# Optimization experiments

Hardware: AMD Instinct MI355X
Metric: run time of the kernel (lower is better)

Reference implementation:

```python
import jax, jax.numpy as jnp
import numpy as np

N = 4096
CIN = 128
COUT = 128
J = 2
DENSITY = 0.01  # ~40 nonzeros per Laplacian row


def _mask(k):
    m = (jax.random.uniform(k, (N, N)) < DENSITY).astype(jnp.float32)
    # Laplacians have nonzero diagonals; also guarantees no empty softmax rows
    return jnp.maximum(m, jnp.eye(N, dtype=jnp.float32))


def setup_inputs() -> dict:
    key = jax.random.key(0)
    ks = jax.random.split(key, 9)
    x = jax.random.normal(ks[0], (N, CIN), dtype=jnp.float32)
    Lup = _mask(ks[1])
    Ldown = _mask(ks[2])
    P = jax.random.normal(ks[3], (N, N), dtype=jnp.float32) / np.float32(np.sqrt(N))
    weight_irr = jax.random.normal(ks[4], (J, CIN, COUT), dtype=jnp.float32) * 0.05
    weight_sol = jax.random.normal(ks[5], (J, CIN, COUT), dtype=jnp.float32) * 0.05
    weight_har = jax.random.normal(ks[6], (CIN, COUT), dtype=jnp.float32) * 0.05
    att_irr = jax.random.normal(ks[7], (2 * J * COUT, 1), dtype=jnp.float32) * 0.05
    att_sol = jax.random.normal(ks[8], (2 * J * COUT, 1), dtype=jnp.float32) * 0.05
    return {"x": x, "Lup": Lup, "Ldown": Ldown, "P": P,
            "weight_irr": weight_irr, "weight_sol": weight_sol,
            "weight_har": weight_har, "att_irr": att_irr, "att_sol": att_sol}


def _masked_row_softmax(e, mask):
    # torch.sparse.softmax over the mask's nonzero pattern, dim=1, then to_dense
    on = mask > 0
    z = jnp.where(on, e, -jnp.inf)
    m = jnp.max(z, axis=1, keepdims=True)
    m = jnp.where(jnp.isfinite(m), m, 0.0)  # guard fully-masked rows
    p = jnp.exp(z - m)                      # exp(-inf)=0 off-pattern
    s = jnp.sum(p, axis=1, keepdims=True)
    s = jnp.where(s == 0, 1.0, s)
    return jnp.where(on, p / s, 0.0)


def _branch(x, weight, att, mask):
    j, cout = weight.shape[0], weight.shape[2]
    att_slice = j * cout
    h = jnp.einsum('ni,jio->jno', x, weight)         # [J, N, Cout]
    hf = h.reshape(-1, att_slice)                    # [N, J*Cout] (row-major, as torch)
    src = hf @ att[:att_slice]                       # [N, 1]
    dst = hf @ att[att_slice:]                       # [N, 1]
    e = jax.nn.leaky_relu(src + dst.T)               # [N, N], slope 0.01 (torch default)
    alpha = _masked_row_softmax(e, mask)             # [N, N]
    powers = [alpha]
    for _ in range(j - 1):
        powers.append(powers[-1] @ alpha)            # iterative matrix powers
    alpha_exp = jnp.stack(powers)                    # [J, N, N]
    # torch.sum with no dim: full reduction to a SCALAR (faithful to source)
    return jnp.sum(jnp.einsum('jnm,jmo->jno', alpha_exp, h))


def reference(x, Lup, Ldown, P, weight_irr, weight_sol, weight_har, att_irr, att_sol):
    z_irr = _branch(x, weight_irr, att_irr, Ldown)   # scalar
    z_sol = _branch(x, weight_sol, att_sol, Lup)     # scalar
    z_har = (P @ x) @ weight_har                     # [N, Cout]
    return z_irr + z_sol + z_har
```

## Files before the change

### kernel.cpp

```cpp
#include <hip/hip_runtime.h>

typedef __attribute__((ext_vector_type(8))) short short8b;
typedef __attribute__((ext_vector_type(4))) float f32x4;

#define NEG_SENTINEL (-1e30f)

constexpr int C_OFF    = 0;
constexpr int C2_OFF   = 8192;
constexpr int SC_OFF   = 16384;
constexpr int FLAG_I   = 16390;
constexpr int ZERO_N   = 16448;
constexpr int V_OFF    = 16448;
constexpr int NP_OFF   = 19008;
constexpr int SRC_OFF  = 100928;
constexpr int RM_OFF   = 117312;
constexpr int RS_OFF   = 125504;
constexpr int XBT_OFF  = 666176;
constexpr int TP_OFF   = 928320;
constexpr int BM_OFF   = 5122624;

__device__ __forceinline__ unsigned short f2bf(float f) {
  unsigned int u = __float_as_uint(f);
  u += 0x7FFFu + ((u >> 16) & 1u);
  return (unsigned short)(u >> 16);
}
__device__ __forceinline__ float bf2f(unsigned short b) {
  return __uint_as_float(((unsigned int)b) << 16);
}
__device__ __forceinline__ float scrub(float v) {
  unsigned int u = __float_as_uint(v);
  return ((u & 0x7F800000u) == 0x7F800000u) ? 0.f : v;
}

__global__ __launch_bounds__(128) void k_vvec(const void* __restrict__ xin,
                                              const void* __restrict__ w_irr,
                                              const void* __restrict__ w_sol,
                                              const void* __restrict__ att_irr,
                                              const void* __restrict__ att_sol,
                                              int* __restrict__ flagp,
                                              float* __restrict__ vvec) {
  __shared__ int sdet[128];
  int t = threadIdx.x;
  unsigned int ef = (((const unsigned int*)xin)[t] >> 7) & 0xFFu;
  sdet[t] = (ef >= 100u && ef <= 150u) ? 1 : 0;
  __syncthreads();
  for (int d = 64; d > 0; d >>= 1) { if (t < d) sdet[t] += sdet[t + d]; __syncthreads(); }
  int f = (sdet[0] >= 96) ? 1 : 0;
  if (blockIdx.x == 0 && t == 0) *flagp = f;
  int bx = blockIdx.x;
  int b = bx / 10, rem = bx % 10, j = rem / 5, tt = rem % 5;
  const void* Wv = (b == 0 ? w_irr : w_sol);
  const void* Av = (b == 0 ? att_irr : att_sol);
  int i = t;
  float s = 0.f;
  if (f) {
    const unsigned short* Wr = (const unsigned short*)Wv + (size_t)j * 16384 + (size_t)i * 128;
    const unsigned short* Ar = (const unsigned short*)Av + tt * 128;
    for (int o = 0; o < 128; o += 8) {
      uint4 wq = *(const uint4*)(Wr + o);
      unsigned int ww[4] = {wq.x, wq.y, wq.z, wq.w};
      float cf[8];
      if (tt < 4) {
        uint4 aq = *(const uint4*)(Ar + o);
        unsigned int aa[4] = {aq.x, aq.y, aq.z, aq.w};
#pragma unroll
        for (int u = 0; u < 4; ++u) {
          cf[2 * u] = bf2f((unsigned short)(aa[u] & 0xFFFFu));
          cf[2 * u + 1] = bf2f((unsigned short)(aa[u] >> 16));
        }
      } else {
#pragma unroll
        for (int e = 0; e < 8; ++e) cf[e] = 1.0f;
      }
#pragma unroll
      for (int u = 0; u < 4; ++u) {
        s += bf2f((unsigned short)(ww[u] & 0xFFFFu)) * cf[2 * u];
        s += bf2f((unsigned short)(ww[u] >> 16)) * cf[2 * u + 1];
      }
    }
  } else {
    const float* Wr = (const float*)Wv + (size_t)j * 16384 + (size_t)i * 128;
    const float* Ar = (const float*)Av + tt * 128;
    for (int o = 0; o < 128; o += 4) {
      float4 wq = *(const float4*)(Wr + o);
      float4 aq = {1.f, 1.f, 1.f, 1.f};
      if (tt < 4) aq = *(const float4*)(Ar + o);
      s += wq.x * aq.x + wq.y * aq.y + wq.z * aq.z + wq.w * aq.w;
    }
  }
  vvec[bx * 128 + i] = s;
}

__global__ __launch_bounds__(256) void k_prep(const void* __restrict__ xin,
                                              const int* __restrict__ flag,
                                              const float* __restrict__ vvec,
                                              unsigned short* __restrict__ xbT,
                                              float* __restrict__ np,
                                              float* __restrict__ srcdst) {
  __shared__ __align__(16) float ldsx[64 * 130];
  __shared__ __align__(16) float ldsv[2560];
  __shared__ float ldsp[4 * 1280];
  __shared__ float npl[1280];
  int f = *flag;
  int t = threadIdx.x, nb = blockIdx.x * 64;
  for (int q = 0; q < 16; ++q) {
    int idx = q * 256 + t;
    int row = idx >> 6, cp = idx & 63;
    float vx, vy;
    if (f) {
      unsigned int u = ((const unsigned int*)xin)[(size_t)(nb + row) * 64 + cp];
      vx = bf2f((unsigned short)(u & 0xFFFFu));
      vy = bf2f((unsigned short)(u >> 16));
    } else {
      float2 v = ((const float2*)xin)[(size_t)(nb + row) * 64 + cp];
      vx = v.x; vy = v.y;
    }
    ldsx[row * 130 + cp * 2] = vx;
    ldsx[row * 130 + cp * 2 + 1] = vy;
  }
  for (int q = 0; q < 10; ++q) { int idx = q * 256 + t; ldsv[idx] = vvec[idx]; }
  __syncthreads();
  for (int q = 0; q < 32; ++q) {
    int idx = q * 256 + t;
    int c = idx >> 6, n = idx & 63;
    xbT[(size_t)c * 4096 + nb + n] = f2bf(ldsx[n * 130 + c]);
  }
  int row = t & 63, qq = t >> 6, i0 = qq * 32;
  float acc[20];
#pragma unroll
  for (int k = 0; k < 20; ++k) acc[k] = 0.f;
  for (int i = i0; i < i0 + 32; i += 2) {
    float2 xv = *(const float2*)&ldsx[row * 130 + i];
#pragma unroll
    for (int k = 0; k < 20; ++k) {
      float2 vk = *(const float2*)&ldsv[k * 128 + i];
      acc[k] += xv.x * vk.x + xv.y * vk.y;
    }
  }
#pragma unroll
  for (int k = 0; k < 20; ++k) ldsp[qq * 1280 + row * 20 + k] = acc[k];
  __syncthreads();
  for (int rep = 0; rep < 5; ++rep) {
    int idx = rep * 256 + t;
    int k = idx >> 6, rr = idx & 63;
    float s = ldsp[rr * 20 + k] + ldsp[1280 + rr * 20 + k] +
              ldsp[2560 + rr * 20 + k] + ldsp[3840 + rr * 20 + k];
    npl[k * 64 + rr] = s;
    np[(size_t)k * 4096 + nb + rr] = s;
  }
  __syncthreads();
  {
    int b = t >> 7, j = (t >> 6) & 1, kind = (t >> 5) & 1, q = t & 31;
    int bl = q * 2;
    int r = j * 2048 + (nb >> 1) + q;
    int kidx = b * 10 + j * 5 + kind * 2;
    float val = npl[kidx * 64 + bl] + npl[(kidx + 1) * 64 + bl + 1];
    srcdst[b * 8192 + kind * 4096 + r] = val;
  }
}

__global__ __launch_bounds__(256) void k_mask(const void* __restrict__ Ldown,
                                              const void* __restrict__ Lup,
                                              const int* __restrict__ flag,
                                              unsigned char* __restrict__ bm) {
  __shared__ __align__(16) unsigned char lb[4096];
  int f = *flag;
  int b = blockIdx.y;
  const void* mask = b ? Lup : Ldown;
  int t = threadIdx.x;
  size_t wg = (size_t)blockIdx.x * 4096;
  if (f) {
    const uint4* in4 = (const uint4*)mask;
#pragma unroll
    for (int k = 0; k < 16; ++k) {
      size_t bi = wg + k * 256 + t;
      uint4 v = in4[bi];
      unsigned int by = 0;
      by |= ((v.x & 0xFFFFu) != 0u ? 1u : 0u) << 0;
      by |= ((v.x >> 16) != 0u ? 1u : 0u) << 1;
      by |= ((v.y & 0xFFFFu) != 0u ? 1u : 0u) << 2;
      by |= ((v.y >> 16) != 0u ? 1u : 0u) << 3;
      by |= ((v.z & 0xFFFFu) != 0u ? 1u : 0u) << 4;
      by |= ((v.z >> 16) != 0u ? 1u : 0u) << 5;
      by |= ((v.w & 0xFFFFu) != 0u ? 1u : 0u) << 6;
      by |= ((v.w >> 16) != 0u ? 1u : 0u) << 7;
      lb[k * 256 + t] = (unsigned char)by;
    }
  } else {
    const uint4* in4 = (const uint4*)mask;
#pragma unroll
    for (int k = 0; k < 16; ++k) {
      size_t bi = wg + k * 256 + t;
      uint4 v0 = in4[2 * bi], v1 = in4[2 * bi + 1];
      unsigned int by = 0;
      by |= (v0.x != 0u ? 1u : 0u) << 0;
      by |= (v0.y != 0u ? 1u : 0u) << 1;
      by |= (v0.z != 0u ? 1u : 0u) << 2;
      by |= (v0.w != 0u ? 1u : 0u) << 3;
      by |= (v1.x != 0u ? 1u : 0u) << 4;
      by |= (v1.y != 0u ? 1u : 0u) << 5;
      by |= (v1.z != 0u ? 1u : 0u) << 6;
      by |= (v1.w != 0u ? 1u : 0u) << 7;
      lb[k * 256 + t] = (unsigned char)by;
    }
  }
  __syncthreads();
  ((uint4*)(bm + (size_t)b * 2097152 + wg))[t] = ((const uint4*)lb)[t];
}

__global__ __launch_bounds__(256) void k_soft(float* __restrict__ ws) {
  const unsigned char* bm = (const unsigned char*)(ws + BM_OFF);
  int b = blockIdx.y, t = threadIdx.x;
  int wid = t >> 6, l = t & 63;
  const float* srcp = ws + SRC_OFF + b * 8192;
  const float* dstp = srcp + 4096;
#pragma unroll
  for (int rr = 0; rr < 2; ++rr) {
    int r = blockIdx.x * 8 + wid * 2 + rr;
    unsigned long long hm =
        ((const unsigned long long*)(bm + ((size_t)b * 4096 + r) * 512))[l];
    float srcr = srcp[r];
    float ev[8];
    int mv[8];
    int nh = 0;
    float mx = NEG_SENTINEL, sm = 0.f;
    unsigned long long mm = hm;
    while (mm) {
      int bit = __builtin_ctzll(mm); mm &= mm - 1;
      int m = l * 64 + bit;
      float e = srcr + dstp[m];
      e = (e >= 0.f) ? e : 0.01f * e;
      if (nh < 8) { ev[nh] = e; mv[nh] = m; }
      ++nh;
      if (e > mx) { sm = sm * __expf(mx - e) + 1.f; mx = e; }
      else        { sm += __expf(e - mx); }
    }
    for (int d = 1; d < 64; d <<= 1) {
      float om = __shfl_xor(mx, d);
      float os = __shfl_xor(sm, d);
      float M = fmaxf(mx, om);
      sm = sm * __expf(mx - M) + os * __expf(om - M);
      mx = M;
    }
    if (l == 0) {
      ws[RM_OFF + b * 4096 + r] = mx;
      ws[RS_OFF + b * 4096 + r] = sm;
    }
    float inv = 1.0f / sm;
    int cap = (nh < 8) ? nh : 8;
    for (int i = 0; i < cap; ++i)
      atomicAdd(&ws[C_OFF + b * 4096 + mv[i]], __expf(ev[i] - mx) * inv);
    if (nh > 8) {
      int skip = 8;
      mm = hm;
      while (mm) {
        int bit = __builtin_ctzll(mm); mm &= mm - 1;
        if (skip > 0) { --skip; continue; }
        int m = l * 64 + bit;
        float e = srcr + dstp[m];
        e = (e >= 0.f) ? e : 0.01f * e;
        atomicAdd(&ws[C_OFF + b * 4096 + m], __expf(e - mx) * inv);
      }
    }
  }
}

__global__ __launch_bounds__(256) void k_c2(float* __restrict__ ws) {
  const unsigned char* bm = (const unsigned char*)(ws + BM_OFF);
  int b = blockIdx.y, t = threadIdx.x;
  int wid = t >> 6, l = t & 63;
  const float* srcp = ws + SRC_OFF + b * 8192;
  const float* dstp = srcp + 4096;
#pragma unroll
  for (int rr = 0; rr < 2; ++rr) {
    int r = blockIdx.x * 8 + wid * 2 + rr;
    unsigned long long hm =
        ((const unsigned long long*)(bm + ((size_t)b * 4096 + r) * 512))[l];
    float srcr = srcp[r];
    float rm = ws[RM_OFF + b * 4096 + r];
    float w = ws[C_OFF + b * 4096 + r] / ws[RS_OFF + b * 4096 + r];
    while (hm) {
      int bit = __builtin_ctzll(hm); hm &= hm - 1;
      int m = l * 64 + bit;
      float e = srcr + dstp[m];
      e = (e >= 0.f) ? e : 0.01f * e;
      atomicAdd(&ws[C2_OFF + b * 4096 + m], __expf(e - rm) * w);
    }
  }
}

__global__ __launch_bounds__(256) void k_scalar(float* __restrict__ ws) {
  int b = blockIdx.x, t = threadIdx.x;
  const float* cb  = ws + C_OFF  + b * 4096;
  const float* c2b = ws + C2_OFF + b * 4096;
  const float* hr0 = ws + NP_OFF + (b * 10 + 4) * 4096;
  const float* hr1 = ws + NP_OFF + (b * 10 + 9) * 4096;
  double acc = 0.0;
  for (int m = t; m < 4096; m += 256)
    acc += (double)scrub(cb[m]) * (double)scrub(hr0[m]) +
           (double)scrub(c2b[m]) * (double)scrub(hr1[m]);
  __shared__ double sd[256];
  sd[t] = acc;
  __syncthreads();
  for (int s = 128; s > 0; s >>= 1) { if (t < s) sd[t] += sd[t + s]; __syncthreads(); }
  if (t == 0) atomicAdd(&ws[SC_OFF], (float)sd[0]);
}

__global__ __launch_bounds__(256) void k_gemm1(const void* __restrict__ P,
                                               const unsigned short* __restrict__ xbT,
                                               const int* __restrict__ flag,
                                               float* __restrict__ TP) {
  __shared__ __align__(16) unsigned short a_lds[64 * 40];
  __shared__ __align__(16) unsigned short b_lds[128 * 40];
  int f = *flag;
  const int mt = blockIdx.x & 63, ks = blockIdx.x >> 6;
  const int mb = mt * 64;
  const int t = threadIdx.x;
  const int w = t >> 6, l = t & 63, quad = l >> 4, lr = l & 15;
  f32x4 acc[8] = {};
  const int arow = t >> 2, akq = (t & 3) << 3;
  const int bn = t >> 1, bh = (t & 1) << 4;
  const int k0 = ks * 512;
  uint4 aU, bU0, bU1;
#define LOADT(IT)                                                              \
  {                                                                            \
    const int kb = k0 + (IT) * 32;                                             \
    if (f) {                                                                   \
      aU = *(const uint4*)((const unsigned short*)P +                          \
                           (size_t)(mb + arow) * 4096 + kb + akq);             \
    } else {                                                                   \
      const float* pa = (const float*)P + (size_t)(mb + arow) * 4096 + kb + akq; \
      float4 f0 = *(const float4*)pa;                                          \
      float4 f1 = *(const float4*)(pa + 4);                                    \
      unsigned short u[8] = {f2bf(f0.x), f2bf(f0.y), f2bf(f0.z), f2bf(f0.w),   \
                             f2bf(f1.x), f2bf(f1.y), f2bf(f1.z), f2bf(f1.w)};  \
      aU = *(const uint4*)u;                                                   \
    }                                                                          \
    const unsigned short* src = xbT + (size_t)bn * 4096 + kb + bh;             \
    bU0 = *(const uint4*)src;                                                  \
    bU1 = *(const uint4*)(src + 8);                                            \
  }
  LOADT(0);
  for (int it = 0; it < 16; ++it) {
    *(uint4*)&a_lds[arow * 40 + akq] = aU;
    *(uint4*)&b_lds[bn * 40 + bh] = bU0;
    *(uint4*)&b_lds[bn * 40 + bh + 8] = bU1;
    __syncthreads();
    if (it < 15) LOADT(it + 1);
    short8b af = *(short8b*)&a_lds[(w * 16 + lr) * 40 + quad * 8];
#pragma unroll
    for (int nt = 0; nt < 8; ++nt) {
      short8b bf = *(short8b*)&b_lds[(nt * 16 + lr) * 40 + quad * 8];
      acc[nt] = __builtin_amdgcn_mfma_f32_16x16x32_bf16(af, bf, acc[nt], 0, 0, 0);
    }
    if (it < 15) __syncthreads();
  }
#undef LOADT
  float* Tp = TP + (size_t)ks * 524288;
#pragma unroll
  for (int nt = 0; nt < 8; ++nt)
#pragma unroll
    for (int rr = 0; rr < 4; ++rr) {
      int row = mb + w * 16 + quad * 4 + rr;
      int col = nt * 16 + lr;
      Tp[(size_t)row * 128 + col] = acc[nt][rr];
    }
}

__global__ __launch_bounds__(256) void k_gemm2(const float* __restrict__ TP,
                                               const void* __restrict__ W,
                                               const float* __restrict__ ws,
                                               void* __restrict__ outv) {
  __shared__ float tl[16 * 128];
  int f = ((const int*)ws)[FLAG_I];
  int t = threadIdx.x;
  int rb = blockIdx.x * 16;
  for (int q = 0; q < 2; ++q) {
    int vi = q * 256 + t;
    size_t base = (size_t)rb * 128 + (size_t)vi * 4;
    float4 s = {0.f, 0.f, 0.f, 0.f};
#pragma unroll
    for (int p = 0; p < 8; ++p) {
      float4 v = *(const float4*)&TP[(size_t)p * 524288 + base];
      s.x += v.x; s.y += v.y; s.z += v.z; s.w += v.w;
    }
    *(float4*)&tl[vi * 4] = s;
  }
  __syncthreads();
  int col = t & 127, rg = t >> 7;
  int r0 = rg * 8;
  float acc[8] = {};
  for (int k = 0; k < 128; k += 4) {
    float w0, w1, w2, w3;
    if (f) {
      const unsigned short* W16 = (const unsigned short*)W;
      w0 = bf2f(W16[(k + 0) * 128 + col]); w1 = bf2f(W16[(k + 1) * 128 + col]);
      w2 = bf2f(W16[(k + 2) * 128 + col]); w3 = bf2f(W16[(k + 3) * 128 + col]);
    } else {
      const float* W32 = (const float*)W;
      w0 = W32[(k + 0) * 128 + col]; w1 = W32[(k + 1) * 128 + col];
      w2 = W32[(k + 2) * 128 + col]; w3 = W32[(k + 3) * 128 + col];
    }
#pragma unroll
    for (int rr = 0; rr < 8; ++rr) {
      float4 tv = *(const float4*)&tl[(r0 + rr) * 128 + k];
      acc[rr] += tv.x * w0 + tv.y * w1 + tv.z * w2 + tv.w * w3;
    }
  }
  float s = scrub(ws[SC_OFF]);
#pragma unroll
  for (int rr = 0; rr < 8; ++rr) {
    size_t oi = (size_t)(rb + r0 + rr) * 128 + col;
    float v = s + acc[rr];
    if (f) ((unsigned short*)outv)[oi] = f2bf(v);
    else   ((float*)outv)[oi] = v;
  }
}

extern "C" void kernel_launch(void* const* d_in, const int* in_sizes, int n_in,
                              void* d_out, int out_size, void* d_ws, size_t ws_size,
                              hipStream_t stream) {
  const void* x       = d_in[0];
  const void* Lup     = d_in[1];
  const void* Ldown   = d_in[2];
  const void* P       = d_in[3];
  const void* w_irr   = d_in[4];
  const void* w_sol   = d_in[5];
  const void* w_har   = d_in[6];
  const void* att_irr = d_in[7];
  const void* att_sol = d_in[8];
  float* ws = (float*)d_ws;

  hipMemsetAsync(d_ws, 0, (size_t)ZERO_N * sizeof(float), stream);
  k_vvec  <<<20, 128, 0, stream>>>(x, w_irr, w_sol, att_irr, att_sol,
                                   (int*)ws + FLAG_I, ws + V_OFF);
  k_prep  <<<64, 256, 0, stream>>>(x, (int*)ws + FLAG_I, ws + V_OFF,
                                   (unsigned short*)(ws + XBT_OFF), ws + NP_OFF,
                                   ws + SRC_OFF);
  k_gemm1 <<<512, 256, 0, stream>>>(P, (const unsigned short*)(ws + XBT_OFF),
                                    (int*)ws + FLAG_I, ws + TP_OFF);
  k_mask  <<<dim3(512, 2), 256, 0, stream>>>(Ldown, Lup, (int*)ws + FLAG_I,
                                             (unsigned char*)(ws + BM_OFF));
  k_soft  <<<dim3(512, 2), 256, 0, stream>>>(ws);
  k_c2    <<<dim3(512, 2), 256, 0, stream>>>(ws);
  k_scalar<<<2, 256, 0, stream>>>(ws);
  k_gemm2 <<<256, 256, 0, stream>>>(ws + TP_OFF, w_har, ws, d_out);
}
```

Baseline: 320.8 us.

## Fuse all stages into one persistent kernel with software grid barriers

```diff
diff --git a/kernel.cpp b/kernel.cpp
--- a/kernel.cpp
+++ b/kernel.cpp
@@ -4,20 +4,23 @@
 typedef __attribute__((ext_vector_type(4))) float f32x4;
 
 #define NEG_SENTINEL (-1e30f)
+#define MAGIC 0x5A17C0DE
+constexpr int NB = 256;
 
 constexpr int C_OFF    = 0;
 constexpr int C2_OFF   = 8192;
-constexpr int SC_OFF   = 16384;
-constexpr int FLAG_I   = 16390;
-constexpr int ZERO_N   = 16448;
+constexpr int BAR_CNT  = 16388;
+constexpr int BAR_GEN  = 16389;
+constexpr int BAR_MAG  = 16390;
 constexpr int V_OFF    = 16448;
 constexpr int NP_OFF   = 19008;
 constexpr int SRC_OFF  = 100928;
 constexpr int RM_OFF   = 117312;
 constexpr int RS_OFF   = 125504;
-constexpr int XBT_OFF  = 666176;
-constexpr int TP_OFF   = 928320;
-constexpr int BM_OFF   = 5122624;
+constexpr int XBT_OFF  = 133696;
+constexpr int T_OFF    = 395840;
+constexpr int TP_OFF   = 920128;
+constexpr int BM_OFF   = 3017280;
 
 __device__ __forceinline__ unsigned short f2bf(float f) {
   unsigned int u = __float_as_uint(f);
@@ -32,417 +35,425 @@
   return ((u & 0x7F800000u) == 0x7F800000u) ? 0.f : v;
 }
 
-__global__ __launch_bounds__(128) void k_vvec(const void* __restrict__ xin,
-                                              const void* __restrict__ w_irr,
-                                              const void* __restrict__ w_sol,
-                                              const void* __restrict__ att_irr,
-                                              const void* __restrict__ att_sol,
-                                              int* __restrict__ flagp,
-                                              float* __restrict__ vvec) {
-  __shared__ int sdet[128];
-  int t = threadIdx.x;
-  unsigned int ef = (((const unsigned int*)xin)[t] >> 7) & 0xFFu;
-  sdet[t] = (ef >= 100u && ef <= 150u) ? 1 : 0;
+__device__ __forceinline__ void gbar(int* ib) {
   __syncthreads();
-  for (int d = 64; d > 0; d >>= 1) { if (t < d) sdet[t] += sdet[t + d]; __syncthreads(); }
-  int f = (sdet[0] >= 96) ? 1 : 0;
-  if (blockIdx.x == 0 && t == 0) *flagp = f;
-  int bx = blockIdx.x;
-  int b = bx / 10, rem = bx % 10, j = rem / 5, tt = rem % 5;
-  const void* Wv = (b == 0 ? w_irr : w_sol);
-  const void* Av = (b == 0 ? att_irr : att_sol);
-  int i = t;
-  float s = 0.f;
-  if (f) {
-    const unsigned short* Wr = (const unsigned short*)Wv + (size_t)j * 16384 + (size_t)i * 128;
-    const unsigned short* Ar = (const unsigned short*)Av + tt * 128;
-    for (int o = 0; o < 128; o += 8) {
-      uint4 wq = *(const uint4*)(Wr + o);
-      unsigned int ww[4] = {wq.x, wq.y, wq.z, wq.w};
-      float cf[8];
-      if (tt < 4) {
-        uint4 aq = *(const uint4*)(Ar + o);
-        unsigned int aa[4] = {aq.x, aq.y, aq.z, aq.w};
+  if (threadIdx.x == 0) {
+    __threadfence();
+    int g = __hip_atomic_load(&ib[BAR_GEN], __ATOMIC_RELAXED, __HIP_MEMORY_SCOPE_AGENT);
+    int a = __hip_atomic_fetch_add(&ib[BAR_CNT], 1, __ATOMIC_ACQ_REL, __HIP_MEMORY_SCOPE_AGENT);
+    if (a == NB - 1) {
+      __hip_atomic_store(&ib[BAR_CNT], 0, __ATOMIC_RELAXED, __HIP_MEMORY_SCOPE_AGENT);
+      __hip_atomic_store(&ib[BAR_GEN], g + 1, __ATOMIC_RELEASE, __HIP_MEMORY_SCOPE_AGENT);
+    } else {
+      while (__hip_atomic_load(&ib[BAR_GEN], __ATOMIC_ACQUIRE, __HIP_MEMORY_SCOPE_AGENT) == g)
+        __builtin_amdgcn_s_sleep(2);
+    }
+  }
+  __syncthreads();
+}
+
+__global__ __launch_bounds__(256, 1) void k_all(
+    const void* __restrict__ x, const void* __restrict__ Lup,
+    const void* __restrict__ Ldown, const void* __restrict__ P,
+    const void* __restrict__ w_irr, const void* __restrict__ w_sol,
+    const void* __restrict__ w_har, const void* __restrict__ att_irr,
+    const void* __restrict__ att_sol, float* __restrict__ ws,
+    void* __restrict__ outv) {
+  __shared__ __align__(16) unsigned char smem[69632];
+  int* ib = (int*)ws;
+  const int bid = blockIdx.x, t = threadIdx.x;
+
+  if (bid == 0 && t == 0) {
+    __hip_atomic_store(&ib[BAR_CNT], 0, __ATOMIC_RELAXED, __HIP_MEMORY_SCOPE_AGENT);
+    __hip_atomic_store(&ib[BAR_GEN], 0, __ATOMIC_RELAXED, __HIP_MEMORY_SCOPE_AGENT);
+    __threadfence();
+    __hip_atomic_store(&ib[BAR_MAG], MAGIC, __ATOMIC_RELEASE, __HIP_MEMORY_SCOPE_AGENT);
+  }
+
+  int flag;
+  {
+    int* sd = (int*)smem;
+    unsigned int ef = (((const unsigned int*)x)[t & 127] >> 7) & 0xFFu;
+    sd[t] = (ef >= 100u && ef <= 150u) ? 1 : 0;
+    __syncthreads();
+    for (int d = 128; d > 0; d >>= 1) { if (t < d) sd[t] += sd[t + d]; __syncthreads(); }
+    flag = (sd[0] >= 192) ? 1 : 0;
+    __syncthreads();
+  }
+
+  if (bid < 20 && t < 128) {
+    int b = bid / 10, rem = bid % 10, j = rem / 5, tt = rem % 5;
+    const void* Wv = (b == 0 ? w_irr : w_sol);
+    const void* Av = (b == 0 ? att_irr : att_sol);
+    float s = 0.f;
+    if (flag) {
+      const unsigned short* Wr = (const unsigned short*)Wv + (size_t)j * 16384 + (size_t)t * 128;
+      const unsigned short* Ar = (const unsigned short*)Av + tt * 128;
+      for (int o = 0; o < 128; o += 8) {
+        uint4 wq = *(const uint4*)(Wr + o);
+        unsigned int ww[4] = {wq.x, wq.y, wq.z, wq.w};
+        float cf[8];
+        if (tt < 4) {
+          uint4 aq = *(const uint4*)(Ar + o);
+          unsigned int aa[4] = {aq.x, aq.y, aq.z, aq.w};
+#pragma unroll
+          for (int u = 0; u < 4; ++u) {
+            cf[2 * u] = bf2f((unsigned short)(aa[u] & 0xFFFFu));
+            cf[2 * u + 1] = bf2f((unsigned short)(aa[u] >> 16));
+          }
+        } else {
+#pragma unroll
+          for (int e = 0; e < 8; ++e) cf[e] = 1.0f;
+        }
 #pragma unroll
         for (int u = 0; u < 4; ++u) {
-          cf[2 * u] = bf2f((unsigned short)(aa[u] & 0xFFFFu));
-          cf[2 * u + 1] = bf2f((unsigned short)(aa[u] >> 16));
+          s += bf2f((unsigned short)(ww[u] & 0xFFFFu)) * cf[2 * u];
+          s += bf2f((unsigned short)(ww[u] >> 16)) * cf[2 * u + 1];
+        }
+      }
+    } else {
+      const float* Wr = (const float*)Wv + (size_t)j * 16384 + (size_t)t * 128;
+      const float* Ar = (const float*)Av + tt * 128;
+      for (int o = 0; o < 128; o += 4) {
+        float4 wq = *(const float4*)(Wr + o);
+        float4 aq = {1.f, 1.f, 1.f, 1.f};
+        if (tt < 4) aq = *(const float4*)(Ar + o);
+        s += wq.x * aq.x + wq.y * aq.y + wq.z * aq.z + wq.w * aq.w;
+      }
+    }
+    ws[V_OFF + bid * 128 + t] = s;
+  }
+  if (bid >= 64 && bid < 128) ws[(bid - 64) * 256 + t] = 0.f;
+
+  if (t == 0) {
+    while (__hip_atomic_load(&ib[BAR_MAG], __ATOMIC_ACQUIRE, __HIP_MEMORY_SCOPE_AGENT) != MAGIC)
+      __builtin_amdgcn_s_sleep(2);
+  }
+  __syncthreads();
+  gbar(ib);
+
+  if (bid < 64) {
+    float* ldsx = (float*)smem;
+    float* ldsv = (float*)(smem + 33280);
+    float* ldsp = (float*)(smem + 43520);
+    float* npl  = (float*)(smem + 64000);
+    int nb = bid * 64;
+    for (int q = 0; q < 16; ++q) {
+      int idx = q * 256 + t;
+      int row = idx >> 6, cp = idx & 63;
+      float vx, vy;
+      if (flag) {
+        unsigned int u = ((const unsigned int*)x)[(size_t)(nb + row) * 64 + cp];
+        vx = bf2f((unsigned short)(u & 0xFFFFu));
+        vy = bf2f((unsigned short)(u >> 16));
+      } else {
+        float2 v = ((const float2*)x)[(size_t)(nb + row) * 64 + cp];
+        vx = v.x; vy = v.y;
+      }
+      ldsx[row * 130 + cp * 2] = vx;
+      ldsx[row * 130 + cp * 2 + 1] = vy;
+    }
+    for (int q = 0; q < 10; ++q) { int idx = q * 256 + t; ldsv[idx] = ws[V_OFF + idx]; }
+    __syncthreads();
+    unsigned short* xbT = (unsigned short*)(ws + XBT_OFF);
+    for (int q = 0; q < 32; ++q) {
+      int idx = q * 256 + t;
+      int c = idx >> 6, n = idx & 63;
+      xbT[(size_t)c * 4096 + nb + n] = f2bf(ldsx[n * 130 + c]);
+    }
+    int row = t & 63, qq = t >> 6, i0 = qq * 32;
+    float acc[20];
+#pragma unroll
+    for (int k = 0; k < 20; ++k) acc[k] = 0.f;
+    for (int i = i0; i < i0 + 32; i += 2) {
+      float2 xv = *(const float2*)&ldsx[row * 130 + i];
+#pragma unroll
+      for (int k = 0; k < 20; ++k) {
+        float2 vk = *(const float2*)&ldsv[k * 128 + i];
+        acc[k] += xv.x * vk.x + xv.y * vk.y;
+      }
+    }
+#pragma unroll
+    for (int k = 0; k < 20; ++k) ldsp[qq * 1280 + row * 20 + k] = acc[k];
+    __syncthreads();
+    for (int rep = 0; rep < 5; ++rep) {
+      int idx = rep * 256 + t;
+      int k = idx >> 6, rr = idx & 63;
+      float s = ldsp[rr * 20 + k] + ldsp[1280 + rr * 20 + k] +
+                ldsp[2560 + rr * 20 + k] + ldsp[3840 + rr * 20 + k];
+      npl[k * 64 + rr] = s;
+      ws[NP_OFF + (size_t)k * 4096 + nb + rr] = s;
+    }
+    __syncthreads();
+    {
+      int b = t >> 7, j = (t >> 6) & 1, kind = (t >> 5) & 1, q = t & 31;
+      int bl = q * 2;
+      int r = j * 2048 + (nb >> 1) + q;
+      int kidx = b * 10 + j * 5 + kind * 2;
+      float val = npl[kidx * 64 + bl] + npl[(kidx + 1) * 64 + bl + 1];
+      ws[SRC_OFF + b * 8192 + kind * 4096 + r] = val;
+    }
+  } else {
+    unsigned char* bm = (unsigned char*)(ws + BM_OFF);
+    for (int u = (bid - 64) * 256 + t; u < 262144; u += 192 * 256) {
+      int mb = u >> 17;
+      int rem = u & 131071;
+      const void* mask = mb ? Lup : Ldown;
+      unsigned int ob[4];
+      if (flag) {
+        const uint4* in4 = (const uint4*)mask + (size_t)rem * 16;
+#pragma unroll
+        for (int w4 = 0; w4 < 4; ++w4) {
+          unsigned int byts = 0;
+#pragma unroll
+          for (int bb = 0; bb < 4; ++bb) {
+            uint4 v = in4[w4 * 4 + bb];
+            unsigned int by = 0;
+            by |= ((v.x & 0xFFFFu) != 0u ? 1u : 0u) << 0;
+            by |= ((v.x >> 16) != 0u ? 1u : 0u) << 1;
+            by |= ((v.y & 0xFFFFu) != 0u ? 1u : 0u) << 2;
+            by |= ((v.y >> 16) != 0u ? 1u : 0u) << 3;
+            by |= ((v.z & 0xFFFFu) != 0u ? 1u : 0u) << 4;
+            by |= ((v.z >> 16) != 0u ? 1u : 0u) << 5;
+            by |= ((v.w & 0xFFFFu) != 0u ? 1u : 0u) << 6;
+            by |= ((v.w >> 16) != 0u ? 1u : 0u) << 7;
+            byts |= by << (8 * bb);
+          }
+          ob[w4] = byts;
         }
       } else {
-#pragma unroll
-        for (int e = 0; e < 8; ++e) cf[e] = 1.0f;
-      }
-#pragma unroll
-      for (int u = 0; u < 4; ++u) {
-        s += bf2f((unsigned short)(ww[u] & 0xFFFFu)) * cf[2 * u];
-        s += bf2f((unsigned short)(ww[u] >> 16)) * cf[2 * u + 1];
-      }
-    }
-  } else {
-    const float* Wr = (const float*)Wv + (size_t)j * 16384 + (size_t)i * 128;
-    const float* Ar = (const float*)Av + tt * 128;
-    for (int o = 0; o < 128; o += 4) {
-      float4 wq = *(const float4*)(Wr + o);
-      float4 aq = {1.f, 1.f, 1.f, 1.f};
-      if (tt < 4) aq = *(const float4*)(Ar + o);
-      s += wq.x * aq.x + wq.y * aq.y + wq.z * aq.z + wq.w * aq.w;
-    }
-  }
-  vvec[bx * 128 + i] = s;
-}
-
-__global__ __launch_bounds__(256) void k_prep(const void* __restrict__ xin,
-                                              const int* __restrict__ flag,
-                                              const float* __restrict__ vvec,
-                                              unsigned short* __restrict__ xbT,
-                                              float* __restrict__ np,
-                                              float* __restrict__ srcdst) {
-  __shared__ __align__(16) float ldsx[64 * 130];
-  __shared__ __align__(16) float ldsv[2560];
-  __shared__ float ldsp[4 * 1280];
-  __shared__ float npl[1280];
-  int f = *flag;
-  int t = threadIdx.x, nb = blockIdx.x * 64;
-  for (int q = 0; q < 16; ++q) {
-    int idx = q * 256 + t;
-    int row = idx >> 6, cp = idx & 63;
-    float vx, vy;
-    if (f) {
-      unsigned int u = ((const unsigned int*)xin)[(size_t)(nb + row) * 64 + cp];
-      vx = bf2f((unsigned short)(u & 0xFFFFu));
-      vy = bf2f((unsigned short)(u >> 16));
-    } else {
-      float2 v = ((const float2*)xin)[(size_t)(nb + row) * 64 + cp];
-      vx = v.x; vy = v.y;
-    }
-    ldsx[row * 130 + cp * 2] = vx;
-    ldsx[row * 130 + cp * 2 + 1] = vy;
-  }
-  for (int q = 0; q < 10; ++q) { int idx = q * 256 + t; ldsv[idx] = vvec[idx]; }
-  __syncthreads();
-  for (int q = 0; q < 32; ++q) {
-    int idx = q * 256 + t;
-    int c = idx >> 6, n = idx & 63;
-    xbT[(size_t)c * 4096 + nb + n] = f2bf(ldsx[n * 130 + c]);
-  }
-  int row = t & 63, qq = t >> 6, i0 = qq * 32;
-  float acc[20];
-#pragma unroll
-  for (int k = 0; k < 20; ++k) acc[k] = 0.f;
-  for (int i = i0; i < i0 + 32; i += 2) {
-    float2 xv = *(const float2*)&ldsx[row * 130 + i];
-#pragma unroll
-    for (int k = 0; k < 20; ++k) {
-      float2 vk = *(const float2*)&ldsv[k * 128 + i];
-      acc[k] += xv.x * vk.x + xv.y * vk.y;
-    }
-  }
-#pragma unroll
-  for (int k = 0; k < 20; ++k) ldsp[qq * 1280 + row * 20 + k] = acc[k];
-  __syncthreads();
-  for (int rep = 0; rep < 5; ++rep) {
-    int idx = rep * 256 + t;
-    int k = idx >> 6, rr = idx & 63;
-    float s = ldsp[rr * 20 + k] + ldsp[1280 + rr * 20 + k] +
-              ldsp[2560 + rr * 20 + k] + ldsp[3840 + rr * 20 + k];
-    npl[k * 64 + rr] = s;
-    np[(size_t)k * 4096 + nb + rr] = s;
-  }
-  __syncthreads();
-  {
-    int b = t >> 7, j = (t >> 6) & 1, kind = (t >> 5) & 1, q = t & 31;
-    int bl = q * 2;
-    int r = j * 2048 + (nb >> 1) + q;
-    int kidx = b * 10 + j * 5 + kind * 2;
-    float val = npl[kidx * 64 + bl] + npl[(kidx + 1) * 64 + bl + 1];
-    srcdst[b * 8192 + kind * 4096 + r] = val;
-  }
-}
-
-__global__ __launch_bounds__(256) void k_mask(const void* __restrict__ Ldown,
-                                              const void* __restrict__ Lup,
-                                              const int* __restrict__ flag,
-                                              unsigned char* __restrict__ bm) {
-  __shared__ __align__(16) unsigned char lb[4096];
-  int f = *flag;
-  int b = blockIdx.y;
-  const void* mask = b ? Lup : Ldown;
-  int t = threadIdx.x;
-  size_t wg = (size_t)blockIdx.x * 4096;
-  if (f) {
-    const uint4* in4 = (const uint4*)mask;
-#pragma unroll
-    for (int k = 0; k < 16; ++k) {
-      size_t bi = wg + k * 256 + t;
-      uint4 v = in4[bi];
-      unsigned int by = 0;
-      by |= ((v.x & 0xFFFFu) != 0u ? 1u : 0u) << 0;
-      by |= ((v.x >> 16) != 0u ? 1u : 0u) << 1;
-      by |= ((v.y & 0xFFFFu) != 0u ? 1u : 0u) << 2;
-      by |= ((v.y >> 16) != 0u ? 1u : 0u) << 3;
-      by |= ((v.z & 0xFFFFu) != 0u ? 1u : 0u) << 4;
-      by |= ((v.z >> 16) != 0u ? 1u : 0u) << 5;
-      by |= ((v.w & 0xFFFFu) != 0u ? 1u : 0u) << 6;
-      by |= ((v.w >> 16) != 0u ? 1u : 0u) << 7;
-      lb[k * 256 + t] = (unsigned char)by;
-    }
-  } else {
-    const uint4* in4 = (const uint4*)mask;
-#pragma unroll
-    for (int k = 0; k < 16; ++k) {
-      size_t bi = wg + k * 256 + t;
-      uint4 v0 = in4[2 * bi], v1 = in4[2 * bi + 1];
-      unsigned int by = 0;
-      by |= (v0.x != 0u ? 1u : 0u) << 0;
-      by |= (v0.y != 0u ? 1u : 0u) << 1;
-      by |= (v0.z != 0u ? 1u : 0u) << 2;
-      by |= (v0.w != 0u ? 1u : 0u) << 3;
-      by |= (v1.x != 0u ? 1u : 0u) << 4;
-      by |= (v1.y != 0u ? 1u : 0u) << 5;
-      by |= (v1.z != 0u ? 1u : 0u) << 6;
-      by |= (v1.w != 0u ? 1u : 0u) << 7;
-      lb[k * 256 + t] = (unsigned char)by;
-    }
-  }
-  __syncthreads();
-  ((uint4*)(bm + (size_t)b * 2097152 + wg))[t] = ((const uint4*)lb)[t];
-}
-
-__global__ __launch_bounds__(256) void k_soft(float* __restrict__ ws) {
-  const unsigned char* bm = (const unsigned char*)(ws + BM_OFF);
-  int b = blockIdx.y, t = threadIdx.x;
-  int wid = t >> 6, l = t & 63;
-  const float* srcp = ws + SRC_OFF + b * 8192;
-  const float* dstp = srcp + 4096;
-#pragma unroll
-  for (int rr = 0; rr < 2; ++rr) {
-    int r = blockIdx.x * 8 + wid * 2 + rr;
-    unsigned long long hm =
-        ((const unsigned long long*)(bm + ((size_t)b * 4096 + r) * 512))[l];
-    float srcr = srcp[r];
-    float ev[8];
-    int mv[8];
-    int nh = 0;
-    float mx = NEG_SENTINEL, sm = 0.f;
-    unsigned long long mm = hm;
-    while (mm) {
-      int bit = __builtin_ctzll(mm); mm &= mm - 1;
-      int m = l * 64 + bit;
-      float e = srcr + dstp[m];
-      e = (e >= 0.f) ? e : 0.01f * e;
-      if (nh < 8) { ev[nh] = e; mv[nh] = m; }
-      ++nh;
-      if (e > mx) { sm = sm * __expf(mx - e) + 1.f; mx = e; }
-      else        { sm += __expf(e - mx); }
-    }
-    for (int d = 1; d < 64; d <<= 1) {
-      float om = __shfl_xor(mx, d);
-      float os = __shfl_xor(sm, d);
-      float M = fmaxf(mx, om);
-      sm = sm * __expf(mx - M) + os * __expf(om - M);
-      mx = M;
-    }
-    if (l == 0) {
-      ws[RM_OFF + b * 4096 + r] = mx;
-      ws[RS_OFF + b * 4096 + r] = sm;
-    }
-    float inv = 1.0f / sm;
-    int cap = (nh < 8) ? nh : 8;
-    for (int i = 0; i < cap; ++i)
-      atomicAdd(&ws[C_OFF + b * 4096 + mv[i]], __expf(ev[i] - mx) * inv);
-    if (nh > 8) {
-      int skip = 8;
-      mm = hm;
+        const uint4* in4 = (const uint4*)mask + (size_t)rem * 32;
+#pragma unroll
+        for (int w4 = 0; w4 < 4; ++w4) {
+          unsigned int byts = 0;
+#pragma unroll
+          for (int bb = 0; bb < 4; ++bb) {
+            uint4 v0 = in4[w4 * 8 + bb * 2], v1 = in4[w4 * 8 + bb * 2 + 1];
+            unsigned int by = (v0.x != 0u ? 1u : 0u) | ((v0.y != 0u ? 1u : 0u) << 1) |
+                              ((v0.z != 0u ? 1u : 0u) << 2) | ((v0.w != 0u ? 1u : 0u) << 3) |
+                              ((v1.x != 0u ? 1u : 0u) << 4) | ((v1.y != 0u ? 1u : 0u) << 5) |
+                              ((v1.z != 0u ? 1u : 0u) << 6) | ((v1.w != 0u ? 1u : 0u) << 7);
+            byts |= by << (8 * bb);
+          }
+          ob[w4] = byts;
+        }
+      }
+      uint4 o; o.x = ob[0]; o.y = ob[1]; o.z = ob[2]; o.w = ob[3];
+      ((uint4*)bm)[u] = o;
+    }
+  }
+  gbar(ib);
+
+  {
+    const unsigned char* bm = (const unsigned char*)(ws + BM_OFF);
+    int wid = t >> 6, l = t & 63;
+    for (int rr = 0; rr < 8; ++rr) {
+      int GR = bid * 32 + wid * 8 + rr;
+      int b = GR >> 12, r = GR & 4095;
+      unsigned long long hm =
+          ((const unsigned long long*)(bm + ((size_t)b * 4096 + r) * 512))[l];
+      const float* srcp = ws + SRC_OFF + b * 8192;
+      const float* dstp = srcp + 4096;
+      float srcr = srcp[r];
+      float ev[8]; int mv[8]; int nh = 0;
+      float mx = NEG_SENTINEL, sm = 0.f;
+      unsigned long long mm = hm;
       while (mm) {
         int bit = __builtin_ctzll(mm); mm &= mm - 1;
-        if (skip > 0) { --skip; continue; }
         int m = l * 64 + bit;
         float e = srcr + dstp[m];
         e = (e >= 0.f) ? e : 0.01f * e;
-        atomicAdd(&ws[C_OFF + b * 4096 + m], __expf(e - mx) * inv);
-      }
-    }
-  }
-}
-
-__global__ __launch_bounds__(256) void k_c2(float* __restrict__ ws) {
-  const unsigned char* bm = (const unsigned char*)(ws + BM_OFF);
-  int b = blockIdx.y, t = threadIdx.x;
-  int wid = t >> 6, l = t & 63;
-  const float* srcp = ws + SRC_OFF + b * 8192;
-  const float* dstp = srcp + 4096;
-#pragma unroll
-  for (int rr = 0; rr < 2; ++rr) {
-    int r = blockIdx.x * 8 + wid * 2 + rr;
-    unsigned long long hm =
-        ((const unsigned long long*)(bm + ((size_t)b * 4096 + r) * 512))[l];
-    float srcr = srcp[r];
-    float rm = ws[RM_OFF + b * 4096 + r];
-    float w = ws[C_OFF + b * 4096 + r] / ws[RS_OFF + b * 4096 + r];
-    while (hm) {
-      int bit = __builtin_ctzll(hm); hm &= hm - 1;
-      int m = l * 64 + bit;
-      float e = srcr + dstp[m];
-      e = (e >= 0.f) ? e : 0.01f * e;
-      atomicAdd(&ws[C2_OFF + b * 4096 + m], __expf(e - rm) * w);
-    }
-  }
-}
-
-__global__ __launch_bounds__(256) void k_scalar(float* __restrict__ ws) {
-  int b = blockIdx.x, t = threadIdx.x;
-  const float* cb  = ws + C_OFF  + b * 4096;
-  const float* c2b = ws + C2_OFF + b * 4096;
-  const float* hr0 = ws + NP_OFF + (b * 10 + 4) * 4096;
-  const float* hr1 = ws + NP_OFF + (b * 10 + 9) * 4096;
-  double acc = 0.0;
-  for (int m = t; m < 4096; m += 256)
-    acc += (double)scrub(cb[m]) * (double)scrub(hr0[m]) +
-           (double)scrub(c2b[m]) * (double)scrub(hr1[m]);
-  __shared__ double sd[256];
-  sd[t] = acc;
+        if (nh < 8) { ev[nh] = e; mv[nh] = m; }
+        ++nh;
+        if (e > mx) { sm = sm * __expf(mx - e) + 1.f; mx = e; }
+        else        { sm += __expf(e - mx); }
+      }
+      for (int d = 1; d < 64; d <<= 1) {
+        float om = __shfl_xor(mx, d);
+        float os = __shfl_xor(sm, d);
+        float M = fmaxf(mx, om);
+        sm = sm * __expf(mx - M) + os * __expf(om - M);
+        mx = M;
+      }
+      if (l == 0) {
+        ws[RM_OFF + b * 4096 + r] = mx;
+        ws[RS_OFF + b * 4096 + r] = sm;
+      }
+      float inv = 1.0f / sm;
+      int cap = (nh < 8) ? nh : 8;
+      for (int i = 0; i < cap; ++i)
+        atomicAdd(&ws[C_OFF + b * 4096 + mv[i]], __expf(ev[i] - mx) * inv);
+      if (nh > 8) {
+        int skip = 8;
+        mm = hm;
+        while (mm) {
+          int bit = __builtin_ctzll(mm); mm &= mm - 1;
+          if (skip > 0) { --skip; continue; }
+          int m = l * 64 + bit;
+          float e = srcr + dstp[m];
+          e = (e >= 0.f) ? e : 0.01f * e;
+          atomicAdd(&ws[C_OFF + b * 4096 + m], __expf(e - mx) * inv);
+        }
+      }
+    }
+  }
   __syncthreads();
-  for (int s = 128; s > 0; s >>= 1) { if (t < s) sd[t] += sd[t + s]; __syncthreads(); }
-  if (t == 0) atomicAdd(&ws[SC_OFF], (float)sd[0]);
-}
-
-__global__ __launch_bounds__(256) void k_gemm1(const void* __restrict__ P,
-                                               const unsigned short* __restrict__ xbT,
-                                               const int* __restrict__ flag,
-                                               float* __restrict__ TP) {
-  __shared__ __align__(16) unsigned short a_lds[64 * 40];
-  __shared__ __align__(16) unsigned short b_lds[128 * 40];
-  int f = *flag;
-  const int mt = blockIdx.x & 63, ks = blockIdx.x >> 6;
-  const int mb = mt * 64;
-  const int t = threadIdx.x;
-  const int w = t >> 6, l = t & 63, quad = l >> 4, lr = l & 15;
-  f32x4 acc[8] = {};
-  const int arow = t >> 2, akq = (t & 3) << 3;
-  const int bn = t >> 1, bh = (t & 1) << 4;
-  const int k0 = ks * 512;
-  uint4 aU, bU0, bU1;
+  {
+    unsigned short* a_lds = (unsigned short*)smem;
+    unsigned short* b_lds = (unsigned short*)(smem + 5120);
+    const unsigned short* xbT = (const unsigned short*)(ws + XBT_OFF);
+    const int mt = bid & 63, ks = bid >> 6;
+    const int mb = mt * 64;
+    const int w = t >> 6, l = t & 63, quad = l >> 4, lr = l & 15;
+    f32x4 acc[8] = {};
+    const int arow = t >> 2, akq = (t & 3) << 3;
+    const int bn = t >> 1, bh = (t & 1) << 4;
+    const int k0 = ks * 1024;
+    uint4 aU, bU0, bU1;
 #define LOADT(IT)                                                              \
   {                                                                            \
     const int kb = k0 + (IT) * 32;                                             \
-    if (f) {                                                                   \
+    if (flag) {                                                                \
       aU = *(const uint4*)((const unsigned short*)P +                          \
                            (size_t)(mb + arow) * 4096 + kb + akq);             \
     } else {                                                                   \
       const float* pa = (const float*)P + (size_t)(mb + arow) * 4096 + kb + akq; \
       float4 f0 = *(const float4*)pa;                                          \
       float4 f1 = *(const float4*)(pa + 4);                                    \
-      unsigned short u[8] = {f2bf(f0.x), f2bf(f0.y), f2bf(f0.z), f2bf(f0.w),   \
-                             f2bf(f1.x), f2bf(f1.y), f2bf(f1.z), f2bf(f1.w)};  \
-      aU = *(const uint4*)u;                                                   \
+      unsigned short uu[8] = {f2bf(f0.x), f2bf(f0.y), f2bf(f0.z), f2bf(f0.w),  \
+                              f2bf(f1.x), f2bf(f1.y), f2bf(f1.z), f2bf(f1.w)}; \
+      aU = *(const uint4*)uu;                                                  \
     }                                                                          \
     const unsigned short* src = xbT + (size_t)bn * 4096 + kb + bh;             \
     bU0 = *(const uint4*)src;                                                  \
     bU1 = *(const uint4*)(src + 8);                                            \
   }
-  LOADT(0);
-  for (int it = 0; it < 16; ++it) {
-    *(uint4*)&a_lds[arow * 40 + akq] = aU;
-    *(uint4*)&b_lds[bn * 40 + bh] = bU0;
-    *(uint4*)&b_lds[bn * 40 + bh + 8] = bU1;
-    __syncthreads();
-    if (it < 15) LOADT(it + 1);
-    short8b af = *(short8b*)&a_lds[(w * 16 + lr) * 40 + quad * 8];
-#pragma unroll
-    for (int nt = 0; nt < 8; ++nt) {
-      short8b bf = *(short8b*)&b_lds[(nt * 16 + lr) * 40 + quad * 8];
-      acc[nt] = __builtin_amdgcn_mfma_f32_16x16x32_bf16(af, bf, acc[nt], 0, 0, 0);
-    }
-    if (it < 15) __syncthreads();
-  }
+    LOADT(0);
+    for (int it = 0; it < 32; ++it) {
+      *(uint4*)&a_lds[arow * 40 + akq] = aU;
+      *(uint4*)&b_lds[bn * 40 + bh] = bU0;
+      *(uint4*)&b_lds[bn * 40 + bh + 8] = bU1;
+      __syncthreads();
+      if (it < 31) LOADT(it + 1);
+      short8b af = *(short8b*)&a_lds[(w * 16 + lr) * 40 + quad * 8];
+#pragma unroll
+      for (int nt = 0; nt < 8; ++nt) {
+        short8b bf = *(short8b*)&b_lds[(nt * 16 + lr) * 40 + quad * 8];
+        acc[nt] = __builtin_amdgcn_mfma_f32_16x16x32_bf16(af, bf, acc[nt], 0, 0, 0);
+      }
+      if (it < 31) __syncthreads();
+    }
 #undef LOADT
-  float* Tp = TP + (size_t)ks * 524288;
-#pragma unroll
-  for (int nt = 0; nt < 8; ++nt)
-#pragma unroll
-    for (int rr = 0; rr < 4; ++rr) {
-      int row = mb + w * 16 + quad * 4 + rr;
-      int col = nt * 16 + lr;
-      Tp[(size_t)row * 128 + col] = acc[nt][rr];
-    }
-}
-
-__global__ __launch_bounds__(256) void k_gemm2(const float* __restrict__ TP,
-                                               const void* __restrict__ W,
-                                               const float* __restrict__ ws,
-                                               void* __restrict__ outv) {
-  __shared__ float tl[16 * 128];
-  int f = ((const int*)ws)[FLAG_I];
-  int t = threadIdx.x;
-  int rb = blockIdx.x * 16;
-  for (int q = 0; q < 2; ++q) {
-    int vi = q * 256 + t;
-    size_t base = (size_t)rb * 128 + (size_t)vi * 4;
-    float4 s = {0.f, 0.f, 0.f, 0.f};
-#pragma unroll
-    for (int p = 0; p < 8; ++p) {
-      float4 v = *(const float4*)&TP[(size_t)p * 524288 + base];
-      s.x += v.x; s.y += v.y; s.z += v.z; s.w += v.w;
-    }
-    *(float4*)&tl[vi * 4] = s;
-  }
-  __syncthreads();
-  int col = t & 127, rg = t >> 7;
-  int r0 = rg * 8;
-  float acc[8] = {};
-  for (int k = 0; k < 128; k += 4) {
-    float w0, w1, w2, w3;
-    if (f) {
-      const unsigned short* W16 = (const unsigned short*)W;
-      w0 = bf2f(W16[(k + 0) * 128 + col]); w1 = bf2f(W16[(k + 1) * 128 + col]);
-      w2 = bf2f(W16[(k + 2) * 128 + col]); w3 = bf2f(W16[(k + 3) * 128 + col]);
-    } else {
-      const float* W32 = (const float*)W;
-      w0 = W32[(k + 0) * 128 + col]; w1 = W32[(k + 1) * 128 + col];
-      w2 = W32[(k + 2) * 128 + col]; w3 = W32[(k + 3) * 128 + col];
-    }
-#pragma unroll
+    float* Tp = ws + TP_OFF + (size_t)ks * 524288;
+#pragma unroll
+    for (int nt = 0; nt < 8; ++nt)
+#pragma unroll
+      for (int rr = 0; rr < 4; ++rr) {
+        int row = mb + w * 16 + quad * 4 + rr;
+        int col = nt * 16 + lr;
+        Tp[(size_t)row * 128 + col] = acc[nt][rr];
+      }
+  }
+  gbar(ib);
+
+  {
+    const unsigned char* bm = (const unsigned char*)(ws + BM_OFF);
+    int wid = t >> 6, l = t & 63;
     for (int rr = 0; rr < 8; ++rr) {
-      float4 tv = *(const float4*)&tl[(r0 + rr) * 128 + k];
-      acc[rr] += tv.x * w0 + tv.y * w1 + tv.z * w2 + tv.w * w3;
-    }
-  }
-  float s = scrub(ws[SC_OFF]);
-#pragma unroll
-  for (int rr = 0; rr < 8; ++rr) {
-    size_t oi = (size_t)(rb + r0 + rr) * 128 + col;
-    float v = s + acc[rr];
-    if (f) ((unsigned short*)outv)[oi] = f2bf(v);
-    else   ((float*)outv)[oi] = v;
+      int GR = bid * 32 + wid * 8 + rr;
+      int b = GR >> 12, r = GR & 4095;
+      unsigned long long hm =
+          ((const unsigned long long*)(bm + ((size_t)b * 4096 + r) * 512))[l];
+      const float* srcp = ws + SRC_OFF + b * 8192;
+      const float* dstp = srcp + 4096;
+      float srcr = srcp[r];
+      float rm = ws[RM_OFF + b * 4096 + r];
+      float w = ws[C_OFF + b * 4096 + r] / ws[RS_OFF + b * 4096 + r];
+      while (hm) {
+        int bit = __builtin_ctzll(hm); hm &= hm - 1;
+        int m = l * 64 + bit;
+        float e = srcr + dstp[m];
+        e = (e >= 0.f) ? e : 0.01f * e;
+        atomicAdd(&ws[C2_OFF + b * 4096 + m], __expf(e - rm) * w);
+      }
+    }
+    const float4* tp = (const float4*)(ws + TP_OFF);
+    float4* T4 = (float4*)(ws + T_OFF);
+    for (int k = t; k < 512; k += 256) {
+      size_t i4 = (size_t)bid * 512 + k;
+      float4 s0 = tp[i4], s1 = tp[131072 + i4], s2 = tp[262144 + i4], s3 = tp[393216 + i4];
+      float4 s;
+      s.x = s0.x + s1.x + s2.x + s3.x;
+      s.y = s0.y + s1.y + s2.y + s3.y;
+      s.z = s0.z + s1.z + s2.z + s3.z;
+      s.w = s0.w + s1.w + s2.w + s3.w;
+      T4[i4] = s;
+    }
+  }
+  gbar(ib);
+
+  float scal;
+  {
+    double* sd = (double*)(smem + 8192);
+    double acc = 0.0;
+    for (int m = t; m < 8192; m += 256) {
+      int b = m >> 12, mm = m & 4095;
+      float c1 = scrub(ws[C_OFF + b * 4096 + mm]);
+      float c2 = scrub(ws[C2_OFF + b * 4096 + mm]);
+      float h0 = scrub(ws[NP_OFF + (b * 10 + 4) * 4096 + mm]);
+      float h1 = scrub(ws[NP_OFF + (b * 10 + 9) * 4096 + mm]);
+      acc += (double)c1 * (double)h0 + (double)c2 * (double)h1;
+    }
+    sd[t] = acc;
+    __syncthreads();
+    for (int s = 128; s > 0; s >>= 1) { if (t < s) sd[t] += sd[t + s]; __syncthreads(); }
+    scal = (float)sd[0];
+    __syncthreads();
+  }
+  {
+    float* tl = (float*)smem;
+    int rb = bid * 16;
+    const float4* T4 = (const float4*)(ws + T_OFF);
+    for (int q = 0; q < 2; ++q) {
+      int vi = q * 256 + t;
+      ((float4*)tl)[vi] = T4[(size_t)rb * 32 + vi];
+    }
+    __syncthreads();
+    int col = t & 127, rg = t >> 7;
+    int r0 = rg * 8;
+    float acc[8] = {};
+    for (int k = 0; k < 128; k += 4) {
+      float w0, w1, w2, w3;
+      if (flag) {
+        const unsigned short* W16 = (const unsigned short*)w_har;
+        w0 = bf2f(W16[(k + 0) * 128 + col]); w1 = bf2f(W16[(k + 1) * 128 + col]);
+        w2 = bf2f(W16[(k + 2) * 128 + col]); w3 = bf2f(W16[(k + 3) * 128 + col]);
+      } else {
+        const float* W32 = (const float*)w_har;
+        w0 = W32[(k + 0) * 128 + col]; w1 = W32[(k + 1) * 128 + col];
+        w2 = W32[(k + 2) * 128 + col]; w3 = W32[(k + 3) * 128 + col];
+      }
+#pragma unroll
+      for (int rr = 0; rr < 8; ++rr) {
+        float4 tv = *(const float4*)&tl[(r0 + rr) * 128 + k];
+        acc[rr] += tv.x * w0 + tv.y * w1 + tv.z * w2 + tv.w * w3;
+      }
+    }
+    float s = scrub(scal);
+#pragma unroll
+    for (int rr = 0; rr < 8; ++rr) {
+      size_t oi = (size_t)(rb + r0 + rr) * 128 + col;
+      float v = s + acc[rr];
+      if (flag) ((unsigned short*)outv)[oi] = f2bf(v);
+      else      ((float*)outv)[oi] = v;
+    }
   }
 }
 
 extern "C" void kernel_launch(void* const* d_in, const int* in_sizes, int n_in,
                               void* d_out, int out_size, void* d_ws, size_t ws_size,
                               hipStream_t stream) {
-  const void* x       = d_in[0];
-  const void* Lup     = d_in[1];
-  const void* Ldown   = d_in[2];
-  const void* P       = d_in[3];
-  const void* w_irr   = d_in[4];
-  const void* w_sol   = d_in[5];
-  const void* w_har   = d_in[6];
-  const void* att_irr = d_in[7];
-  const void* att_sol = d_in[8];
-  float* ws = (float*)d_ws;
-
-  hipMemsetAsync(d_ws, 0, (size_t)ZERO_N * sizeof(float), stream);
-  k_vvec  <<<20, 128, 0, stream>>>(x, w_irr, w_sol, att_irr, att_sol,
-                                   (int*)ws + FLAG_I, ws + V_OFF);
-  k_prep  <<<64, 256, 0, stream>>>(x, (int*)ws + FLAG_I, ws + V_OFF,
-                                   (unsigned short*)(ws + XBT_OFF), ws + NP_OFF,
-                                   ws + SRC_OFF);
-  k_gemm1 <<<512, 256, 0, stream>>>(P, (const unsigned short*)(ws + XBT_OFF),
-                                    (int*)ws + FLAG_I, ws + TP_OFF);
-  k_mask  <<<dim3(512, 2), 256, 0, stream>>>(Ldown, Lup, (int*)ws + FLAG_I,
-                                             (unsigned char*)(ws + BM_OFF));
-  k_soft  <<<dim3(512, 2), 256, 0, stream>>>(ws);
-  k_c2    <<<dim3(512, 2), 256, 0, stream>>>(ws);
-  k_scalar<<<2, 256, 0, stream>>>(ws);
-  k_gemm2 <<<256, 256, 0, stream>>>(ws + TP_OFF, w_har, ws, d_out);
-}
+  k_all<<<NB, 256, 0, stream>>>(d_in[0], d_in[1], d_in[2], d_in[3], d_in[4],
+                                d_in[5], d_in[6], d_in[7], d_in[8],
+                                (float*)d_ws, d_out);
+}
```

Measured after the change: 473.5 us. 1.48x slower.
